# Kernel optimization log

Measured on AMD Instinct MI355X. Metric: run time of the kernel, lower is better.

Reference implementation:

```python
import jax, jax.numpy as jnp
import numpy as np

GRID_SIZE = 5
SPLINE_ORDER = 3
EPS = 1e-5


def make_grid(in_features):
    # efficient-kan: grid_range=[-1,1], points from -order..grid_size+order
    h = 2.0 / GRID_SIZE
    g = jnp.arange(-SPLINE_ORDER, GRID_SIZE + SPLINE_ORDER + 1, dtype=jnp.float32) * h - 1.0
    return jnp.tile(g[None, :], (in_features, 1))  # [in, grid_size + 2*order + 1]


def b_splines(x, grid):
    # x: [B, in], grid: [in, G] -> bases: [B, in, grid_size + order]
    xg = x[:, :, None]
    bases = ((xg >= grid[:, :-1]) & (xg < grid[:, 1:])).astype(x.dtype)
    for k in range(1, SPLINE_ORDER + 1):
        left = (xg - grid[:, : -(k + 1)]) / (grid[:, k:-1] - grid[:, : -(k + 1)])
        right = (grid[:, k + 1:] - xg) / (grid[:, k + 1:] - grid[:, 1:-k])
        bases = left * bases[:, :, :-1] + right * bases[:, :, 1:]
    return bases


def kan_linear(x, grid, base_w, spline_w, spline_scaler):
    # base path: silu(x) @ base_w.T ; spline path: bsplines(x) contracted with scaled spline weight
    base_out = jnp.einsum('bi,oi->bo', jax.nn.silu(x), base_w)
    bases = b_splines(x, grid)  # [B, in, C]
    sw = spline_w * spline_scaler[:, :, None]  # [out, in, C]
    spline_out = jnp.einsum('bic,oic->bo', bases, sw)
    return base_out + spline_out


def layer_norm(x, w, b):
    mu = jnp.mean(x, axis=-1, keepdims=True)
    var = jnp.mean(jnp.square(x - mu), axis=-1, keepdims=True)
    return (x - mu) * jax.lax.rsqrt(var + EPS) * w + b


def setup_inputs() -> dict:
    key = jax.random.key(0)
    ks = jax.random.split(key, 8)
    B, F, H, E = 65536, 32, 64, 64
    OUT = E * F  # 2048
    C = GRID_SIZE + SPLINE_ORDER  # 8 coeffs per edge
    x = jax.random.normal(ks[0], (B, F), dtype=jnp.float32)
    return {
        'x': x,
        'ln_w': jnp.ones((F,), jnp.float32),
        'ln_b': jnp.zeros((F,), jnp.float32),
        'bw1': jax.random.normal(ks[1], (H, F), jnp.float32) * 0.1,
        'sw1': jax.random.normal(ks[2], (H, F, C), jnp.float32) * 0.1,
        'ss1': jax.random.normal(ks[3], (H, F), jnp.float32) * 0.1 + 1.0,
        'bw2': jax.random.normal(ks[4], (OUT, H), jnp.float32) * 0.1,
        'sw2': jax.random.normal(ks[5], (OUT, H, C), jnp.float32) * 0.1,
        'ss2': jax.random.normal(ks[6], (OUT, H), jnp.float32) * 0.1 + 1.0,
        'grid1': make_grid(F),
        'grid2': make_grid(H),
    }


def reference(x, ln_w, ln_b, bw1, sw1, ss1, bw2, sw2, ss2, grid1, grid2):
    h = layer_norm(x, ln_w, ln_b)
    h = kan_linear(h, grid1, bw1, sw1, ss1)   # [B, 64]
    out = kan_linear(h, grid2, bw2, sw2, ss2)  # [B, 2048]
    return out
```

## Files before the change

### kernel.cpp

```cpp
#include <hip/hip_runtime.h>
#include <stdint.h>

#define BATCH   65536
#define FIN     32
#define HID     64
#define NOUT    2048
#define NC      8
#define NF      9
#define K1      288
#define K2      576

#define BM      256
#define BN      256
#define BK      32
#define KT      18
#define NBUF    4

typedef __bf16 bf16x8 __attribute__((ext_vector_type(8)));
typedef float f32x4 __attribute__((ext_vector_type(4)));

__device__ __forceinline__ uint16_t f2bf(float f) {
    uint32_t u = __builtin_bit_cast(uint32_t, f);
    uint32_t r = (u + 0x7fffu + ((u >> 16) & 1u)) >> 16;
    return (uint16_t)r;
}
__device__ __forceinline__ float silu_f(float v) {
    return v / (1.f + __expf(-v));
}

__device__ __forceinline__ void bspline8u(float xv, float out[8]) {
    float s = (xv + 2.2f) * 2.5f;
    int c = (int)floorf(s);
    float gc = (float)(c - 3) * 0.4f - 1.0f;
    float u = (xv - gc) * 2.5f;
    float u1 = 1.f - u;
    float uu = u * u, u3 = uu * u;
    float w0 = u1 * u1 * u1 * (1.f / 6.f);
    float w1 = (3.f * u3 - 6.f * uu + 4.f) * (1.f / 6.f);
    float w2 = (-3.f * u3 + 3.f * uu + 3.f * u + 1.f) * (1.f / 6.f);
    float w3 = u3 * (1.f / 6.f);
#pragma unroll
    for (int t = 0; t < 8; t++) {
        int d = c - t;
        out[t] = (d == 0) ? w3 : (d == 1) ? w2 : (d == 2) ? w1 : (d == 3) ? w0 : 0.f;
    }
}

__global__ void pack_w1(const float* __restrict__ bw1, const float* __restrict__ sw1,
                        const float* __restrict__ ss1, uint16_t* __restrict__ w1L) {
    int idx = blockIdx.x * 256 + threadIdx.x;
    if (idx >= 64 * K1) return;
    int o = idx / K1, k = idx % K1;
    int i = k / 9, j = k % 9;
    float v = (j == 0) ? bw1[o * FIN + i]
                       : sw1[(o * FIN + i) * NC + (j - 1)] * ss1[o * FIN + i];
    w1L[idx] = f2bf(v);
}

__global__ void pack_w2(const float* __restrict__ bw2, const float* __restrict__ sw2,
                        const float* __restrict__ ss2, uint16_t* __restrict__ w2p) {
    int idx = blockIdx.x * 256 + threadIdx.x;
    if (idx >= NOUT * K2) return;
    int n = idx / K2, k = idx % K2;
    int j = k >> 6, i = k & 63;
    float v = (j == 0) ? bw2[n * HID + i]
                       : sw2[(n * HID + i) * NC + (j - 1)] * ss2[n * HID + i];
    w2p[idx] = f2bf(v);
}

#define FBR   64
#define A1LD  296
__global__ __launch_bounds__(256) void featurize(
    const float* __restrict__ x, const float* __restrict__ lnw, const float* __restrict__ lnb,
    const uint16_t* __restrict__ w1L, uint16_t* __restrict__ a2) {

    __shared__ __align__(16) uint16_t w1s[64 * A1LD];
    __shared__ __align__(16) uint16_t a1s[FBR * A1LD];

    const int tid = threadIdx.x;
    const int wv = tid >> 6, lane = tid & 63;
    const int rowBase = blockIdx.x * FBR;

#pragma unroll
    for (int t = 0; t < 9; ++t) {
        int idx = t * 256 + tid;
        int o = idx / 36, cc = idx % 36;
        uint4 v = *(const uint4*)(w1L + idx * 8);
        *(uint4*)&w1s[o * A1LD + cc * 8] = v;
    }

    const int prow = tid >> 2, pq = tid & 3;
    const float* xp = x + (size_t)(rowBase + prow) * FIN + pq * 8;
    float xv[8];
    *(float4*)&xv[0] = ((const float4*)xp)[0];
    *(float4*)&xv[4] = ((const float4*)xp)[1];
    float s = 0.f, s2 = 0.f;
#pragma unroll
    for (int j = 0; j < 8; j++) { s += xv[j]; s2 += xv[j] * xv[j]; }
    s += __shfl_xor(s, 1);  s2 += __shfl_xor(s2, 1);
    s += __shfl_xor(s, 2);  s2 += __shfl_xor(s2, 2);
    const float mu = s * (1.f / 32.f);
    const float var = s2 * (1.f / 32.f) - mu * mu;
    const float rstd = rsqrtf(var + 1e-5f);

    float wl[8], bl[8];
    *(float4*)&wl[0] = ((const float4*)(lnw + pq * 8))[0];
    *(float4*)&wl[4] = ((const float4*)(lnw + pq * 8))[1];
    *(float4*)&bl[0] = ((const float4*)(lnb + pq * 8))[0];
    *(float4*)&bl[4] = ((const float4*)(lnb + pq * 8))[1];

    __align__(16) uint16_t tmp[72];
#pragma unroll
    for (int ii = 0; ii < 8; ii++) {
        float xn = (xv[ii] - mu) * rstd * wl[ii] + bl[ii];
        tmp[ii * 9] = f2bf(silu_f(xn));
        float bs[8];
        bspline8u(xn, bs);
#pragma unroll
        for (int j = 0; j < 8; j++) tmp[ii * 9 + 1 + j] = f2bf(bs[j]);
    }
    {
        uint16_t* dst = &a1s[prow * A1LD + pq * 72];
#pragma unroll
        for (int q = 0; q < 9; q++) *(uint4*)(dst + q * 8) = *(const uint4*)&tmp[q * 8];
    }
    __syncthreads();

    f32x4 acc[4];
#pragma unroll
    for (int n = 0; n < 4; n++) acc[n] = (f32x4){0.f, 0.f, 0.f, 0.f};
    const int arow = wv * 16 + (lane & 15);
    const int koff = (lane >> 4) * 8;
#pragma unroll
    for (int ks = 0; ks < 9; ++ks) {
        bf16x8 af = *(const bf16x8*)&a1s[arow * A1LD + ks * 32 + koff];
#pragma unroll
        for (int n = 0; n < 4; n++) {
            bf16x8 bv = *(const bf16x8*)&w1s[(n * 16 + (lane & 15)) * A1LD + ks * 32 + koff];
            acc[n] = __builtin_amdgcn_mfma_f32_16x16x32_bf16(af, bv, acc[n], 0, 0, 0);
        }
    }

    const int r0 = wv * 16 + ((lane >> 4) << 2);
    const int cb = lane & 15;
#pragma unroll
    for (int n = 0; n < 4; n++)
#pragma unroll
        for (int r = 0; r < 4; r++) {
            float h = acc[n][r];
            float o9[9];
            o9[0] = silu_f(h);
            bspline8u(h, &o9[1]);
            uint16_t* op = a2 + (size_t)(rowBase + r0 + r) * K2 + n * 16 + cb;
#pragma unroll
            for (int j = 0; j < 9; j++) op[j * 64] = f2bf(o9[j]);
        }
}

__device__ __forceinline__ void gload16(const uint16_t* g, const uint16_t* l) {
    __builtin_amdgcn_global_load_lds(
        (const __attribute__((address_space(1))) void*)g,
        (__attribute__((address_space(3))) void*)l, 16, 0, 0);
}

__global__ __launch_bounds__(512, 2) void gemm2_kernel(const uint16_t* __restrict__ A,
                                                       const uint16_t* __restrict__ Bt,
                                                       float* __restrict__ C) {
    __shared__ __align__(16) uint16_t lds[NBUF][2][BM * BK];

    const int tid = threadIdx.x;
    const int wv = tid >> 6, lane = tid & 63;
    const int wr = wv >> 2, wc = wv & 3;

    const uint32_t bid = blockIdx.x;
    const uint32_t wk = (bid & 7u) * 256u + (bid >> 3);
    const uint32_t ntile = wk & 7u, mtile = wk >> 3;

    const int srow = tid >> 2;
    const int scol = (((tid & 3) ^ ((tid >> 3) & 3)) << 3);
    const uint16_t* gA = A  + (size_t)(mtile * BM + srow) * K2 + scol;
    const uint16_t* gB = Bt + (size_t)(ntile * BN + srow) * K2 + scol;

#define STAGE_A(b, kt) do { \
    gload16(gA + (kt) * BK,                    &lds[b][0][wv * 512]); \
    gload16(gA + (size_t)128 * K2 + (kt) * BK, &lds[b][0][4096 + wv * 512]); } while (0)
#define STAGE_B(b, kt) do { \
    gload16(gB + (kt) * BK,                    &lds[b][1][wv * 512]); \
    gload16(gB + (size_t)128 * K2 + (kt) * BK, &lds[b][1][4096 + wv * 512]); } while (0)

    const int slot8 = (((lane >> 4) ^ ((lane >> 1) & 3)) << 3);
    const int aoff = (wr * 128 + (lane & 15)) * BK + slot8;
    const int boff = (wc * 64  + (lane & 15)) * BK + slot8;

    f32x4 acc[8][4];
#pragma unroll
    for (int m = 0; m < 8; m++)
#pragma unroll
        for (int n = 0; n < 4; n++) acc[m][n] = (f32x4){0.f, 0.f, 0.f, 0.f};

    STAGE_A(0, 0); STAGE_B(0, 0);
    STAGE_A(1, 1); STAGE_B(1, 1);
    STAGE_A(2, 2); STAGE_B(2, 2);
    asm volatile("s_waitcnt vmcnt(8)" ::: "memory");
    asm volatile("s_barrier" ::: "memory");

    bf16x8 bvc[4];
#pragma unroll
    for (int n = 0; n < 4; ++n) bvc[n] = *(const bf16x8*)&lds[0][1][boff + n * 512];

#pragma unroll
    for (int t = 0; t < KT; ++t) {
        const int b = t & 3;
        bf16x8 afc[4], afB[4], bvn[4];

#pragma unroll
        for (int m = 0; m < 4; ++m) afc[m] = *(const bf16x8*)&lds[b][0][aoff + m * 512];
#pragma unroll
        for (int m = 0; m < 4; ++m) afB[m] = *(const bf16x8*)&lds[b][0][aoff + (m + 4) * 512];
        if (t + 3 < KT) STAGE_A((t + 3) & 3, t + 3);
        if (t <= KT - 4)      asm volatile("s_waitcnt vmcnt(6)" ::: "memory");
        else if (t == KT - 3) asm volatile("s_waitcnt vmcnt(4)" ::: "memory");
        else if (t == KT - 2) asm volatile("s_waitcnt vmcnt(0)" ::: "memory");
        asm volatile("s_barrier" ::: "memory");

        __builtin_amdgcn_s_setprio(1);
#pragma unroll
        for (int m = 0; m < 4; ++m)
#pragma unroll
            for (int n = 0; n < 4; ++n)
                acc[m][n] = __builtin_amdgcn_mfma_f32_16x16x32_bf16(afc[m], bvc[n], acc[m][n], 0, 0, 0);
        __builtin_amdgcn_s_setprio(0);
        asm volatile("s_barrier" ::: "memory");

        if (t < KT - 1) {
#pragma unroll
            for (int n = 0; n < 4; ++n)
                bvn[n] = *(const bf16x8*)&lds[(t + 1) & 3][1][boff + n * 512];
        }
        if (t + 3 < KT) STAGE_B((t + 3) & 3, t + 3);
        asm volatile("s_barrier" ::: "memory");

        __builtin_amdgcn_s_setprio(1);
#pragma unroll
        for (int m = 0; m < 4; ++m)
#pragma unroll
            for (int n = 0; n < 4; ++n)
                acc[m + 4][n] = __builtin_amdgcn_mfma_f32_16x16x32_bf16(afB[m], bvc[n], acc[m + 4][n], 0, 0, 0);
        __builtin_amdgcn_s_setprio(0);

        if (t < KT - 1) {
            asm volatile("s_barrier" ::: "memory");
#pragma unroll
            for (int n = 0; n < 4; ++n) bvc[n] = bvn[n];
        }
    }
#undef STAGE_A
#undef STAGE_B

    const int crow0 = (int)mtile * BM + wr * 128 + ((lane >> 4) << 2);
    const int ccol0 = (int)ntile * BN + wc * 64 + (lane & 15);
#pragma unroll
    for (int m = 0; m < 8; ++m)
#pragma unroll
        for (int n = 0; n < 4; ++n) {
            float* cp = C + (size_t)(crow0 + m * 16) * NOUT + ccol0 + n * 16;
#pragma unroll
            for (int r = 0; r < 4; ++r) cp[(size_t)r * NOUT] = acc[m][n][r];
        }
}

extern "C" void kernel_launch(void* const* d_in, const int* in_sizes, int n_in,
                              void* d_out, int out_size, void* d_ws, size_t ws_size,
                              hipStream_t stream) {
    const float* x    = (const float*)d_in[0];
    const float* lnw  = (const float*)d_in[1];
    const float* lnb  = (const float*)d_in[2];
    const float* bw1  = (const float*)d_in[3];
    const float* sw1  = (const float*)d_in[4];
    const float* ss1  = (const float*)d_in[5];
    const float* bw2  = (const float*)d_in[6];
    const float* sw2  = (const float*)d_in[7];
    const float* ss2  = (const float*)d_in[8];

    char* ws = (char*)d_ws;
    uint16_t* w1L = (uint16_t*)ws;
    uint16_t* w2p = (uint16_t*)(ws + 65536);
    uint16_t* a2  = (uint16_t*)(ws + 65536 + 2359296);
    float* out = (float*)d_out;

    pack_w1<<<dim3(72), dim3(256), 0, stream>>>(bw1, sw1, ss1, w1L);
    pack_w2<<<dim3((NOUT * K2 + 255) / 256), dim3(256), 0, stream>>>(bw2, sw2, ss2, w2p);
    featurize<<<dim3(BATCH / FBR), dim3(256), 0, stream>>>(x, lnw, lnb, w1L, a2);
    gemm2_kernel<<<dim3((BATCH / BM) * (NOUT / BN)), dim3(512), 0, stream>>>(a2, w2p, out);
}
```

Measured before the change: 282.4 us.

## Stage featurize output through LDS and rework GEMM into four interleaved MFMA phases

The featurize kernel now writes its second-layer features into a shared-memory tile that reuses the weight buffer, then copies whole rows to global memory with 16-byte stores instead of scattered 2-byte stores. The GEMM main loop is split into four phases per K-step. Each phase loads two A fragments, issues one global-to-LDS load, and runs eight MFMAs. The B-fragment double buffering in registers is removed to cut register pressure. This adds more barriers and lgkmcnt waits per iteration, which could stall the MFMA pipe.

```diff
diff --git a/kernel.cpp b/kernel.cpp
--- a/kernel.cpp
+++ b/kernel.cpp
@@ -68,14 +68,17 @@
     w2p[idx] = f2bf(v);
 }
 
-#define FBR   64
-#define A1LD  296
+#define FBR    64
+#define A1LD   296
+#define S2LD   584
 __global__ __launch_bounds__(256) void featurize(
     const float* __restrict__ x, const float* __restrict__ lnw, const float* __restrict__ lnb,
     const uint16_t* __restrict__ w1L, uint16_t* __restrict__ a2) {
 
-    __shared__ __align__(16) uint16_t w1s[64 * A1LD];
-    __shared__ __align__(16) uint16_t a1s[FBR * A1LD];
+    __shared__ __align__(16) char fsm[75776];
+    uint16_t* w1s = (uint16_t*)fsm;
+    uint16_t* a1s = (uint16_t*)(fsm + 37888);
+    uint16_t* s2  = (uint16_t*)fsm;
 
     const int tid = threadIdx.x;
     const int wv = tid >> 6, lane = tid & 63;
@@ -94,13 +97,13 @@
     float xv[8];
     *(float4*)&xv[0] = ((const float4*)xp)[0];
     *(float4*)&xv[4] = ((const float4*)xp)[1];
-    float s = 0.f, s2 = 0.f;
-#pragma unroll
-    for (int j = 0; j < 8; j++) { s += xv[j]; s2 += xv[j] * xv[j]; }
-    s += __shfl_xor(s, 1);  s2 += __shfl_xor(s2, 1);
-    s += __shfl_xor(s, 2);  s2 += __shfl_xor(s2, 2);
+    float s = 0.f, s2v = 0.f;
+#pragma unroll
+    for (int j = 0; j < 8; j++) { s += xv[j]; s2v += xv[j] * xv[j]; }
+    s += __shfl_xor(s, 1);  s2v += __shfl_xor(s2v, 1);
+    s += __shfl_xor(s, 2);  s2v += __shfl_xor(s2v, 2);
     const float mu = s * (1.f / 32.f);
-    const float var = s2 * (1.f / 32.f) - mu * mu;
+    const float var = s2v * (1.f / 32.f) - mu * mu;
     const float rstd = rsqrtf(var + 1e-5f);
 
     float wl[8], bl[8];
@@ -140,6 +143,7 @@
             acc[n] = __builtin_amdgcn_mfma_f32_16x16x32_bf16(af, bv, acc[n], 0, 0, 0);
         }
     }
+    __syncthreads();
 
     const int r0 = wv * 16 + ((lane >> 4) << 2);
     const int cb = lane & 15;
@@ -151,10 +155,19 @@
             float o9[9];
             o9[0] = silu_f(h);
             bspline8u(h, &o9[1]);
-            uint16_t* op = a2 + (size_t)(rowBase + r0 + r) * K2 + n * 16 + cb;
+            uint16_t* op = &s2[(size_t)(r0 + r) * S2LD + n * 16 + cb];
 #pragma unroll
             for (int j = 0; j < 9; j++) op[j * 64] = f2bf(o9[j]);
         }
+    __syncthreads();
+
+#pragma unroll
+    for (int q = 0; q < 18; ++q) {
+        int g = q * 256 + tid;
+        int row = g / 72, c = g % 72;
+        uint4 v = *(const uint4*)&s2[row * S2LD + c * 8];
+        *(uint4*)(a2 + (size_t)(rowBase + row) * K2 + c * 8) = v;
+    }
 }
 
 __device__ __forceinline__ void gload16(const uint16_t* g, const uint16_t* l) {
@@ -181,13 +194,6 @@
     const uint16_t* gA = A  + (size_t)(mtile * BM + srow) * K2 + scol;
     const uint16_t* gB = Bt + (size_t)(ntile * BN + srow) * K2 + scol;
 
-#define STAGE_A(b, kt) do { \
-    gload16(gA + (kt) * BK,                    &lds[b][0][wv * 512]); \
-    gload16(gA + (size_t)128 * K2 + (kt) * BK, &lds[b][0][4096 + wv * 512]); } while (0)
-#define STAGE_B(b, kt) do { \
-    gload16(gB + (kt) * BK,                    &lds[b][1][wv * 512]); \
-    gload16(gB + (size_t)128 * K2 + (kt) * BK, &lds[b][1][4096 + wv * 512]); } while (0)
-
     const int slot8 = (((lane >> 4) ^ ((lane >> 1) & 3)) << 3);
     const int aoff = (wr * 128 + (lane & 15)) * BK + slot8;
     const int boff = (wc * 64  + (lane & 15)) * BK + slot8;
@@ -198,64 +204,91 @@
 #pragma unroll
         for (int n = 0; n < 4; n++) acc[m][n] = (f32x4){0.f, 0.f, 0.f, 0.f};
 
-    STAGE_A(0, 0); STAGE_B(0, 0);
-    STAGE_A(1, 1); STAGE_B(1, 1);
-    STAGE_A(2, 2); STAGE_B(2, 2);
+#define ST_A0(b, kt) gload16(gA + (kt) * BK,                    &lds[b][0][wv * 512])
+#define ST_A1(b, kt) gload16(gA + (size_t)128 * K2 + (kt) * BK, &lds[b][0][4096 + wv * 512])
+#define ST_B0(b, kt) gload16(gB + (kt) * BK,                    &lds[b][1][wv * 512])
+#define ST_B1(b, kt) gload16(gB + (size_t)128 * K2 + (kt) * BK, &lds[b][1][4096 + wv * 512])
+
+    ST_A0(0, 0); ST_A1(0, 0); ST_B0(0, 0); ST_B1(0, 0);
+    ST_A0(1, 1); ST_A1(1, 1); ST_B0(1, 1); ST_B1(1, 1);
+    ST_A0(2, 2); ST_A1(2, 2); ST_B0(2, 2); ST_B1(2, 2);
     asm volatile("s_waitcnt vmcnt(8)" ::: "memory");
     asm volatile("s_barrier" ::: "memory");
 
-    bf16x8 bvc[4];
-#pragma unroll
-    for (int n = 0; n < 4; ++n) bvc[n] = *(const bf16x8*)&lds[0][1][boff + n * 512];
-
 #pragma unroll
     for (int t = 0; t < KT; ++t) {
         const int b = t & 3;
-        bf16x8 afc[4], afB[4], bvn[4];
-
-#pragma unroll
-        for (int m = 0; m < 4; ++m) afc[m] = *(const bf16x8*)&lds[b][0][aoff + m * 512];
-#pragma unroll
-        for (int m = 0; m < 4; ++m) afB[m] = *(const bf16x8*)&lds[b][0][aoff + (m + 4) * 512];
-        if (t + 3 < KT) STAGE_A((t + 3) & 3, t + 3);
-        if (t <= KT - 4)      asm volatile("s_waitcnt vmcnt(6)" ::: "memory");
+        const int nb = (t + 3) & 3;
+        const bool st = (t + 3 < KT);
+        const uint16_t* As = &lds[b][0][0];
+        const uint16_t* Bs = &lds[b][1][0];
+        bf16x8 bv[4], aa, ab;
+
+#pragma unroll
+        for (int n = 0; n < 4; ++n) bv[n] = *(const bf16x8*)&Bs[boff + n * 512];
+        aa = *(const bf16x8*)&As[aoff];
+        ab = *(const bf16x8*)&As[aoff + 512];
+        if (st) ST_A0(nb, t + 3);
+        asm volatile("s_barrier" ::: "memory");
+        asm volatile("s_waitcnt lgkmcnt(0)" ::: "memory");
+        __builtin_amdgcn_sched_barrier(0);
+        __builtin_amdgcn_s_setprio(1);
+#pragma unroll
+        for (int n = 0; n < 4; ++n) acc[0][n] = __builtin_amdgcn_mfma_f32_16x16x32_bf16(aa, bv[n], acc[0][n], 0, 0, 0);
+#pragma unroll
+        for (int n = 0; n < 4; ++n) acc[1][n] = __builtin_amdgcn_mfma_f32_16x16x32_bf16(ab, bv[n], acc[1][n], 0, 0, 0);
+        __builtin_amdgcn_s_setprio(0);
+        asm volatile("s_barrier" ::: "memory");
+
+        aa = *(const bf16x8*)&As[aoff + 2 * 512];
+        ab = *(const bf16x8*)&As[aoff + 3 * 512];
+        if (st) ST_A1(nb, t + 3);
+        asm volatile("s_barrier" ::: "memory");
+        asm volatile("s_waitcnt lgkmcnt(0)" ::: "memory");
+        __builtin_amdgcn_sched_barrier(0);
+        __builtin_amdgcn_s_setprio(1);
+#pragma unroll
+        for (int n = 0; n < 4; ++n) acc[2][n] = __builtin_amdgcn_mfma_f32_16x16x32_bf16(aa, bv[n], acc[2][n], 0, 0, 0);
+#pragma unroll
+        for (int n = 0; n < 4; ++n) acc[3][n] = __builtin_amdgcn_mfma_f32_16x16x32_bf16(ab, bv[n], acc[3][n], 0, 0, 0);
+        __builtin_amdgcn_s_setprio(0);
+        asm volatile("s_barrier" ::: "memory");
+
+        aa = *(const bf16x8*)&As[aoff + 4 * 512];
+        ab = *(const bf16x8*)&As[aoff + 5 * 512];
+        if (st) ST_B0(nb, t + 3);
+        asm volatile("s_barrier" ::: "memory");
+        asm volatile("s_waitcnt lgkmcnt(0)" ::: "memory");
+        __builtin_amdgcn_sched_barrier(0);
+        __builtin_amdgcn_s_setprio(1);
+#pragma unroll
+        for (int n = 0; n < 4; ++n) acc[4][n] = __builtin_amdgcn_mfma_f32_16x16x32_bf16(aa, bv[n], acc[4][n], 0, 0, 0);
+#pragma unroll
+        for (int n = 0; n < 4; ++n) acc[5][n] = __builtin_amdgcn_mfma_f32_16x16x32_bf16(ab, bv[n], acc[5][n], 0, 0, 0);
+        __builtin_amdgcn_s_setprio(0);
+        asm volatile("s_barrier" ::: "memory");
+
+        aa = *(const bf16x8*)&As[aoff + 6 * 512];
+        ab = *(const bf16x8*)&As[aoff + 7 * 512];
+        if (st) ST_B1(nb, t + 3);
+        asm volatile("s_barrier" ::: "memory");
+        asm volatile("s_waitcnt lgkmcnt(0)" ::: "memory");
+        __builtin_amdgcn_sched_barrier(0);
+        __builtin_amdgcn_s_setprio(1);
+#pragma unroll
+        for (int n = 0; n < 4; ++n) acc[6][n] = __builtin_amdgcn_mfma_f32_16x16x32_bf16(aa, bv[n], acc[6][n], 0, 0, 0);
+#pragma unroll
+        for (int n = 0; n < 4; ++n) acc[7][n] = __builtin_amdgcn_mfma_f32_16x16x32_bf16(ab, bv[n], acc[7][n], 0, 0, 0);
+        __builtin_amdgcn_s_setprio(0);
+        if (t <= KT - 4)      asm volatile("s_waitcnt vmcnt(8)" ::: "memory");
         else if (t == KT - 3) asm volatile("s_waitcnt vmcnt(4)" ::: "memory");
         else if (t == KT - 2) asm volatile("s_waitcnt vmcnt(0)" ::: "memory");
-        asm volatile("s_barrier" ::: "memory");
-
-        __builtin_amdgcn_s_setprio(1);
-#pragma unroll
-        for (int m = 0; m < 4; ++m)
-#pragma unroll
-            for (int n = 0; n < 4; ++n)
-                acc[m][n] = __builtin_amdgcn_mfma_f32_16x16x32_bf16(afc[m], bvc[n], acc[m][n], 0, 0, 0);
-        __builtin_amdgcn_s_setprio(0);
-        asm volatile("s_barrier" ::: "memory");
-
-        if (t < KT - 1) {
-#pragma unroll
-            for (int n = 0; n < 4; ++n)
-                bvn[n] = *(const bf16x8*)&lds[(t + 1) & 3][1][boff + n * 512];
-        }
-        if (t + 3 < KT) STAGE_B((t + 3) & 3, t + 3);
-        asm volatile("s_barrier" ::: "memory");
-
-        __builtin_amdgcn_s_setprio(1);
-#pragma unroll
-        for (int m = 0; m < 4; ++m)
-#pragma unroll
-            for (int n = 0; n < 4; ++n)
-                acc[m + 4][n] = __builtin_amdgcn_mfma_f32_16x16x32_bf16(afB[m], bvc[n], acc[m + 4][n], 0, 0, 0);
-        __builtin_amdgcn_s_setprio(0);
-
-        if (t < KT - 1) {
-            asm volatile("s_barrier" ::: "memory");
-#pragma unroll
-            for (int n = 0; n < 4; ++n) bvc[n] = bvn[n];
-        }
-    }
-#undef STAGE_A
-#undef STAGE_B
+        if (t < KT - 1) asm volatile("s_barrier" ::: "memory");
+    }
+#undef ST_A0
+#undef ST_A1
+#undef ST_B0
+#undef ST_B1
 
     const int crow0 = (int)mtile * BM + wr * 128 + ((lane >> 4) << 2);
     const int ccol0 = (int)ntile * BN + wc * 64 + (lane & 15);
```

New measurement: 291.6 us. +3.3%, slower.

## Quantize second-layer GEMM to int8 with per-row and per-column scales

Applied to the files above, without the earlier changes.

Replaces the bf16 second GEMM with an int8 MFMA GEMM (16x16x64 i8), quantizing weights per output column and activations per batch row using max-abs scaling. The activation quantization is fused into featurize and goes through LDS to produce coalesced int8 stores. Scales are applied in the epilogue. This halves operand bytes and doubles MFMA throughput per instruction, but int8 quantization of spline/silu features may exceed the accuracy tolerance.

```diff
diff --git a/kernel.cpp b/kernel.cpp
--- a/kernel.cpp
+++ b/kernel.cpp
@@ -10,14 +10,12 @@
 #define K1      288
 #define K2      576
 
-#define BM      256
-#define BN      256
-#define BK      32
-#define KT      18
-#define NBUF    4
+#define BKI     64
+#define KTI     9
 
 typedef __bf16 bf16x8 __attribute__((ext_vector_type(8)));
 typedef float f32x4 __attribute__((ext_vector_type(4)));
+typedef int   i32x4 __attribute__((ext_vector_type(4)));
 
 __device__ __forceinline__ uint16_t f2bf(float f) {
     uint32_t u = __builtin_bit_cast(uint32_t, f);
@@ -57,25 +55,41 @@
     w1L[idx] = f2bf(v);
 }
 
-__global__ void pack_w2(const float* __restrict__ bw2, const float* __restrict__ sw2,
-                        const float* __restrict__ ss2, uint16_t* __restrict__ w2p) {
-    int idx = blockIdx.x * 256 + threadIdx.x;
-    if (idx >= NOUT * K2) return;
-    int n = idx / K2, k = idx % K2;
-    int j = k >> 6, i = k & 63;
-    float v = (j == 0) ? bw2[n * HID + i]
-                       : sw2[(n * HID + i) * NC + (j - 1)] * ss2[n * HID + i];
-    w2p[idx] = f2bf(v);
-}
-
-#define FBR   64
-#define A1LD  296
+__global__ void pack_w2i(const float* __restrict__ bw2, const float* __restrict__ sw2,
+                         const float* __restrict__ ss2, int8_t* __restrict__ w2i,
+                         float* __restrict__ sb) {
+    int gid = blockIdx.x * 256 + threadIdx.x;
+    int o = gid >> 6, lane = gid & 63;
+    float v[9];
+    float mx = 1e-20f;
+#pragma unroll
+    for (int j = 0; j < 9; j++) {
+        int k = lane * 9 + j;
+        int jj = k >> 6, i = k & 63;
+        v[j] = (jj == 0) ? bw2[o * HID + i]
+                         : sw2[(o * HID + i) * NC + (jj - 1)] * ss2[o * HID + i];
+        mx = fmaxf(mx, fabsf(v[j]));
+    }
+#pragma unroll
+    for (int m = 1; m < 64; m <<= 1) mx = fmaxf(mx, __shfl_xor(mx, m));
+    float qs = 127.f / mx;
+    if (lane == 0) sb[o] = mx * (1.f / 127.f);
+#pragma unroll
+    for (int j = 0; j < 9; j++)
+        w2i[(size_t)o * K2 + lane * 9 + j] = (int8_t)(int)rintf(v[j] * qs);
+}
+
+#define FBR    64
+#define A1LD   296
+#define S2BLD  592
 __global__ __launch_bounds__(256) void featurize(
     const float* __restrict__ x, const float* __restrict__ lnw, const float* __restrict__ lnb,
-    const uint16_t* __restrict__ w1L, uint16_t* __restrict__ a2) {
-
-    __shared__ __align__(16) uint16_t w1s[64 * A1LD];
-    __shared__ __align__(16) uint16_t a1s[FBR * A1LD];
+    const uint16_t* __restrict__ w1L, int8_t* __restrict__ a2i, float* __restrict__ sa) {
+
+    __shared__ __align__(16) char fsm[75776];
+    uint16_t* w1s = (uint16_t*)fsm;
+    uint16_t* a1s = (uint16_t*)(fsm + 37888);
+    int8_t*   s2b = (int8_t*)fsm;
 
     const int tid = threadIdx.x;
     const int wv = tid >> 6, lane = tid & 63;
@@ -94,13 +108,13 @@
     float xv[8];
     *(float4*)&xv[0] = ((const float4*)xp)[0];
     *(float4*)&xv[4] = ((const float4*)xp)[1];
-    float s = 0.f, s2 = 0.f;
-#pragma unroll
-    for (int j = 0; j < 8; j++) { s += xv[j]; s2 += xv[j] * xv[j]; }
-    s += __shfl_xor(s, 1);  s2 += __shfl_xor(s2, 1);
-    s += __shfl_xor(s, 2);  s2 += __shfl_xor(s2, 2);
+    float s = 0.f, s2v = 0.f;
+#pragma unroll
+    for (int j = 0; j < 8; j++) { s += xv[j]; s2v += xv[j] * xv[j]; }
+    s += __shfl_xor(s, 1);  s2v += __shfl_xor(s2v, 1);
+    s += __shfl_xor(s, 2);  s2v += __shfl_xor(s2v, 2);
     const float mu = s * (1.f / 32.f);
-    const float var = s2 * (1.f / 32.f) - mu * mu;
+    const float var = s2v * (1.f / 32.f) - mu * mu;
     const float rstd = rsqrtf(var + 1e-5f);
 
     float wl[8], bl[8];
@@ -140,9 +154,11 @@
             acc[n] = __builtin_amdgcn_mfma_f32_16x16x32_bf16(af, bv, acc[n], 0, 0, 0);
         }
     }
+    __syncthreads();
 
     const int r0 = wv * 16 + ((lane >> 4) << 2);
     const int cb = lane & 15;
+    float rmax[4] = {1e-20f, 1e-20f, 1e-20f, 1e-20f};
 #pragma unroll
     for (int n = 0; n < 4; n++)
 #pragma unroll
@@ -151,22 +167,57 @@
             float o9[9];
             o9[0] = silu_f(h);
             bspline8u(h, &o9[1]);
-            uint16_t* op = a2 + (size_t)(rowBase + r0 + r) * K2 + n * 16 + cb;
-#pragma unroll
-            for (int j = 0; j < 9; j++) op[j * 64] = f2bf(o9[j]);
-        }
-}
-
-__device__ __forceinline__ void gload16(const uint16_t* g, const uint16_t* l) {
+            float mx = fabsf(o9[0]);
+#pragma unroll
+            for (int j = 1; j < 9; j++) mx = fmaxf(mx, fabsf(o9[j]));
+            rmax[r] = fmaxf(rmax[r], mx);
+        }
+#pragma unroll
+    for (int m = 1; m < 16; m <<= 1)
+#pragma unroll
+        for (int r = 0; r < 4; r++) rmax[r] = fmaxf(rmax[r], __shfl_xor(rmax[r], m));
+    float qs[4];
+#pragma unroll
+    for (int r = 0; r < 4; r++) qs[r] = 127.f / rmax[r];
+    if (cb == 0)
+#pragma unroll
+        for (int r = 0; r < 4; r++) sa[rowBase + r0 + r] = rmax[r] * (1.f / 127.f);
+
+#pragma unroll
+    for (int n = 0; n < 4; n++)
+#pragma unroll
+        for (int r = 0; r < 4; r++) {
+            float h = acc[n][r];
+            float o9[9];
+            o9[0] = silu_f(h);
+            bspline8u(h, &o9[1]);
+            int8_t* op = &s2b[(r0 + r) * S2BLD + n * 16 + cb];
+#pragma unroll
+            for (int j = 0; j < 9; j++) op[j * 64] = (int8_t)(int)rintf(o9[j] * qs[r]);
+        }
+    __syncthreads();
+
+#pragma unroll
+    for (int q = 0; q < 9; ++q) {
+        int g = q * 256 + tid;
+        int row = g / 36, c = g % 36;
+        uint4 v = *(const uint4*)&s2b[row * S2BLD + c * 16];
+        *(uint4*)(a2i + (size_t)(rowBase + row) * K2 + c * 16) = v;
+    }
+}
+
+__device__ __forceinline__ void gload16(const void* g, const void* l) {
     __builtin_amdgcn_global_load_lds(
         (const __attribute__((address_space(1))) void*)g,
         (__attribute__((address_space(3))) void*)l, 16, 0, 0);
 }
 
-__global__ __launch_bounds__(512, 2) void gemm2_kernel(const uint16_t* __restrict__ A,
-                                                       const uint16_t* __restrict__ Bt,
-                                                       float* __restrict__ C) {
-    __shared__ __align__(16) uint16_t lds[NBUF][2][BM * BK];
+__global__ __launch_bounds__(512, 2) void gemm2i(const int8_t* __restrict__ A,
+                                                 const int8_t* __restrict__ Bt,
+                                                 const float* __restrict__ sa,
+                                                 const float* __restrict__ sb,
+                                                 float* __restrict__ C) {
+    __shared__ __align__(16) int8_t lds[4][2][256 * BKI];
 
     const int tid = threadIdx.x;
     const int wv = tid >> 6, lane = tid & 63;
@@ -177,26 +228,26 @@
     const uint32_t ntile = wk & 7u, mtile = wk >> 3;
 
     const int srow = tid >> 2;
-    const int scol = (((tid & 3) ^ ((tid >> 3) & 3)) << 3);
-    const uint16_t* gA = A  + (size_t)(mtile * BM + srow) * K2 + scol;
-    const uint16_t* gB = Bt + (size_t)(ntile * BN + srow) * K2 + scol;
+    const int scol = (((tid & 3) ^ ((tid >> 4) & 3)) << 4);
+    const int8_t* gA = A  + (size_t)(mtile * 256 + srow) * K2 + scol;
+    const int8_t* gB = Bt + (size_t)(ntile * 256 + srow) * K2 + scol;
 
 #define STAGE_A(b, kt) do { \
-    gload16(gA + (kt) * BK,                    &lds[b][0][wv * 512]); \
-    gload16(gA + (size_t)128 * K2 + (kt) * BK, &lds[b][0][4096 + wv * 512]); } while (0)
+    gload16(gA + (kt) * BKI,                    &lds[b][0][wv * 1024]); \
+    gload16(gA + (size_t)128 * K2 + (kt) * BKI, &lds[b][0][8192 + wv * 1024]); } while (0)
 #define STAGE_B(b, kt) do { \
-    gload16(gB + (kt) * BK,                    &lds[b][1][wv * 512]); \
-    gload16(gB + (size_t)128 * K2 + (kt) * BK, &lds[b][1][4096 + wv * 512]); } while (0)
-
-    const int slot8 = (((lane >> 4) ^ ((lane >> 1) & 3)) << 3);
-    const int aoff = (wr * 128 + (lane & 15)) * BK + slot8;
-    const int boff = (wc * 64  + (lane & 15)) * BK + slot8;
-
-    f32x4 acc[8][4];
+    gload16(gB + (kt) * BKI,                    &lds[b][1][wv * 1024]); \
+    gload16(gB + (size_t)128 * K2 + (kt) * BKI, &lds[b][1][8192 + wv * 1024]); } while (0)
+
+    const int slot16 = (((lane >> 4) ^ ((lane >> 2) & 3)) << 4);
+    const int aoff = (wr * 128 + (lane & 15)) * BKI + slot16;
+    const int boff = (wc * 64  + (lane & 15)) * BKI + slot16;
+
+    i32x4 acc[8][4];
 #pragma unroll
     for (int m = 0; m < 8; m++)
 #pragma unroll
-        for (int n = 0; n < 4; n++) acc[m][n] = (f32x4){0.f, 0.f, 0.f, 0.f};
+        for (int n = 0; n < 4; n++) acc[m][n] = (i32x4){0, 0, 0, 0};
 
     STAGE_A(0, 0); STAGE_B(0, 0);
     STAGE_A(1, 1); STAGE_B(1, 1);
@@ -204,23 +255,23 @@
     asm volatile("s_waitcnt vmcnt(8)" ::: "memory");
     asm volatile("s_barrier" ::: "memory");
 
-    bf16x8 bvc[4];
-#pragma unroll
-    for (int n = 0; n < 4; ++n) bvc[n] = *(const bf16x8*)&lds[0][1][boff + n * 512];
-
-#pragma unroll
-    for (int t = 0; t < KT; ++t) {
+    i32x4 bvc[4];
+#pragma unroll
+    for (int n = 0; n < 4; ++n) bvc[n] = *(const i32x4*)&lds[0][1][boff + n * 1024];
+
+#pragma unroll
+    for (int t = 0; t < KTI; ++t) {
         const int b = t & 3;
-        bf16x8 afc[4], afB[4], bvn[4];
-
-#pragma unroll
-        for (int m = 0; m < 4; ++m) afc[m] = *(const bf16x8*)&lds[b][0][aoff + m * 512];
-#pragma unroll
-        for (int m = 0; m < 4; ++m) afB[m] = *(const bf16x8*)&lds[b][0][aoff + (m + 4) * 512];
-        if (t + 3 < KT) STAGE_A((t + 3) & 3, t + 3);
-        if (t <= KT - 4)      asm volatile("s_waitcnt vmcnt(6)" ::: "memory");
-        else if (t == KT - 3) asm volatile("s_waitcnt vmcnt(4)" ::: "memory");
-        else if (t == KT - 2) asm volatile("s_waitcnt vmcnt(0)" ::: "memory");
+        i32x4 afc[4], afB[4], bvn[4];
+
+#pragma unroll
+        for (int m = 0; m < 4; ++m) afc[m] = *(const i32x4*)&lds[b][0][aoff + m * 1024];
+#pragma unroll
+        for (int m = 0; m < 4; ++m) afB[m] = *(const i32x4*)&lds[b][0][aoff + (m + 4) * 1024];
+        if (t + 3 < KTI) STAGE_A((t + 3) & 3, t + 3);
+        if (t <= KTI - 4)      asm volatile("s_waitcnt vmcnt(6)" ::: "memory");
+        else if (t == KTI - 3) asm volatile("s_waitcnt vmcnt(4)" ::: "memory");
+        else if (t == KTI - 2) asm volatile("s_waitcnt vmcnt(0)" ::: "memory");
         asm volatile("s_barrier" ::: "memory");
 
         __builtin_amdgcn_s_setprio(1);
@@ -228,16 +279,16 @@
         for (int m = 0; m < 4; ++m)
 #pragma unroll
             for (int n = 0; n < 4; ++n)
-                acc[m][n] = __builtin_amdgcn_mfma_f32_16x16x32_bf16(afc[m], bvc[n], acc[m][n], 0, 0, 0);
+                acc[m][n] = __builtin_amdgcn_mfma_i32_16x16x64_i8(afc[m], bvc[n], acc[m][n], 0, 0, 0);
         __builtin_amdgcn_s_setprio(0);
         asm volatile("s_barrier" ::: "memory");
 
-        if (t < KT - 1) {
+        if (t < KTI - 1) {
 #pragma unroll
             for (int n = 0; n < 4; ++n)
-                bvn[n] = *(const bf16x8*)&lds[(t + 1) & 3][1][boff + n * 512];
-        }
-        if (t + 3 < KT) STAGE_B((t + 3) & 3, t + 3);
+                bvn[n] = *(const i32x4*)&lds[(t + 1) & 3][1][boff + n * 1024];
+        }
+        if (t + 3 < KTI) STAGE_B((t + 3) & 3, t + 3);
         asm volatile("s_barrier" ::: "memory");
 
         __builtin_amdgcn_s_setprio(1);
@@ -245,10 +296,10 @@
         for (int m = 0; m < 4; ++m)
 #pragma unroll
             for (int n = 0; n < 4; ++n)
-                acc[m + 4][n] = __builtin_amdgcn_mfma_f32_16x16x32_bf16(afB[m], bvc[n], acc[m + 4][n], 0, 0, 0);
+                acc[m + 4][n] = __builtin_amdgcn_mfma_i32_16x16x64_i8(afB[m], bvc[n], acc[m + 4][n], 0, 0, 0);
         __builtin_amdgcn_s_setprio(0);
 
-        if (t < KT - 1) {
+        if (t < KTI - 1) {
             asm volatile("s_barrier" ::: "memory");
 #pragma unroll
             for (int n = 0; n < 4; ++n) bvc[n] = bvn[n];
@@ -257,16 +308,24 @@
 #undef STAGE_A
 #undef STAGE_B
 
-    const int crow0 = (int)mtile * BM + wr * 128 + ((lane >> 4) << 2);
-    const int ccol0 = (int)ntile * BN + wc * 64 + (lane & 15);
-#pragma unroll
-    for (int m = 0; m < 8; ++m)
+    const int crow0 = (int)mtile * 256 + wr * 128 + ((lane >> 4) << 2);
+    const int ccol0 = (int)ntile * 256 + wc * 64 + (lane & 15);
+    float sbv[4];
+#pragma unroll
+    for (int n = 0; n < 4; ++n) sbv[n] = sb[ccol0 + n * 16];
+#pragma unroll
+    for (int m = 0; m < 8; ++m) {
+        float sav[4];
+#pragma unroll
+        for (int r = 0; r < 4; ++r) sav[r] = sa[crow0 + m * 16 + r];
 #pragma unroll
         for (int n = 0; n < 4; ++n) {
             float* cp = C + (size_t)(crow0 + m * 16) * NOUT + ccol0 + n * 16;
 #pragma unroll
-            for (int r = 0; r < 4; ++r) cp[(size_t)r * NOUT] = acc[m][n][r];
-        }
+            for (int r = 0; r < 4; ++r)
+                cp[(size_t)r * NOUT] = (float)acc[m][n][r] * sav[r] * sbv[n];
+        }
+    }
 }
 
 extern "C" void kernel_launch(void* const* d_in, const int* in_sizes, int n_in,
@@ -284,12 +343,14 @@
 
     char* ws = (char*)d_ws;
     uint16_t* w1L = (uint16_t*)ws;
-    uint16_t* w2p = (uint16_t*)(ws + 65536);
-    uint16_t* a2  = (uint16_t*)(ws + 65536 + 2359296);
+    int8_t*   w2i = (int8_t*)(ws + 65536);
+    float*    sb  = (float*)(ws + 1310720);
+    float*    sa  = (float*)(ws + 1376256);
+    int8_t*   a2i = (int8_t*)(ws + 1703936);
     float* out = (float*)d_out;
 
     pack_w1<<<dim3(72), dim3(256), 0, stream>>>(bw1, sw1, ss1, w1L);
-    pack_w2<<<dim3((NOUT * K2 + 255) / 256), dim3(256), 0, stream>>>(bw2, sw2, ss2, w2p);
-    featurize<<<dim3(BATCH / FBR), dim3(256), 0, stream>>>(x, lnw, lnb, w1L, a2);
-    gemm2_kernel<<<dim3((BATCH / BM) * (NOUT / BN)), dim3(512), 0, stream>>>(a2, w2p, out);
-}
+    pack_w2i<<<dim3(NOUT / 4), dim3(256), 0, stream>>>(bw2, sw2, ss2, w2i, sb);
+    featurize<<<dim3(BATCH / FBR), dim3(256), 0, stream>>>(x, lnw, lnb, w1L, a2i, sa);
+    gemm2i<<<dim3((BATCH / 256) * (NOUT / 256)), dim3(512), 0, stream>>>(a2i, w2i, sa, sb, out);
+}
```

New measurement: 378.7 us. 34.1% more time.

## Switch GEMM to 32x32x16 MFMA and stage featurize output through LDS

Applied to the files above, without the earlier changes.

The main GEMM now uses 32x32x16 bf16 MFMA tiles with 16-float accumulators instead of 16x16x32. This cuts LDS fragment reads per MFMA and simplifies the barrier and prefetch schedule by dropping the B-fragment double buffering. Featurize now writes its second-layer activations into shared memory and copies them out as coalesced 16-byte row stores instead of scattered 2-byte global writes. The costs are an extra LDS round trip and barriers in featurize, and a more strided accumulator store pattern in the GEMM epilogue.

```diff
diff --git a/kernel.cpp b/kernel.cpp
--- a/kernel.cpp
+++ b/kernel.cpp
@@ -10,14 +10,12 @@
 #define K1      288
 #define K2      576
 
-#define BM      256
-#define BN      256
 #define BK      32
 #define KT      18
-#define NBUF    4
 
 typedef __bf16 bf16x8 __attribute__((ext_vector_type(8)));
-typedef float f32x4 __attribute__((ext_vector_type(4)));
+typedef float f32x4  __attribute__((ext_vector_type(4)));
+typedef float f32x16 __attribute__((ext_vector_type(16)));
 
 __device__ __forceinline__ uint16_t f2bf(float f) {
     uint32_t u = __builtin_bit_cast(uint32_t, f);
@@ -68,14 +66,17 @@
     w2p[idx] = f2bf(v);
 }
 
-#define FBR   64
-#define A1LD  296
+#define FBR    64
+#define A1LD   296
+#define S2LD   584
 __global__ __launch_bounds__(256) void featurize(
     const float* __restrict__ x, const float* __restrict__ lnw, const float* __restrict__ lnb,
     const uint16_t* __restrict__ w1L, uint16_t* __restrict__ a2) {
 
-    __shared__ __align__(16) uint16_t w1s[64 * A1LD];
-    __shared__ __align__(16) uint16_t a1s[FBR * A1LD];
+    __shared__ __align__(16) char fsm[75776];
+    uint16_t* w1s = (uint16_t*)fsm;
+    uint16_t* a1s = (uint16_t*)(fsm + 37888);
+    uint16_t* s2  = (uint16_t*)fsm;
 
     const int tid = threadIdx.x;
     const int wv = tid >> 6, lane = tid & 63;
@@ -94,13 +95,13 @@
     float xv[8];
     *(float4*)&xv[0] = ((const float4*)xp)[0];
     *(float4*)&xv[4] = ((const float4*)xp)[1];
-    float s = 0.f, s2 = 0.f;
-#pragma unroll
-    for (int j = 0; j < 8; j++) { s += xv[j]; s2 += xv[j] * xv[j]; }
-    s += __shfl_xor(s, 1);  s2 += __shfl_xor(s2, 1);
-    s += __shfl_xor(s, 2);  s2 += __shfl_xor(s2, 2);
+    float s = 0.f, s2v = 0.f;
+#pragma unroll
+    for (int j = 0; j < 8; j++) { s += xv[j]; s2v += xv[j] * xv[j]; }
+    s += __shfl_xor(s, 1);  s2v += __shfl_xor(s2v, 1);
+    s += __shfl_xor(s, 2);  s2v += __shfl_xor(s2v, 2);
     const float mu = s * (1.f / 32.f);
-    const float var = s2 * (1.f / 32.f) - mu * mu;
+    const float var = s2v * (1.f / 32.f) - mu * mu;
     const float rstd = rsqrtf(var + 1e-5f);
 
     float wl[8], bl[8];
@@ -140,6 +141,7 @@
             acc[n] = __builtin_amdgcn_mfma_f32_16x16x32_bf16(af, bv, acc[n], 0, 0, 0);
         }
     }
+    __syncthreads();
 
     const int r0 = wv * 16 + ((lane >> 4) << 2);
     const int cb = lane & 15;
@@ -151,10 +153,19 @@
             float o9[9];
             o9[0] = silu_f(h);
             bspline8u(h, &o9[1]);
-            uint16_t* op = a2 + (size_t)(rowBase + r0 + r) * K2 + n * 16 + cb;
+            uint16_t* op = &s2[(size_t)(r0 + r) * S2LD + n * 16 + cb];
 #pragma unroll
             for (int j = 0; j < 9; j++) op[j * 64] = f2bf(o9[j]);
         }
+    __syncthreads();
+
+#pragma unroll
+    for (int q = 0; q < 18; ++q) {
+        int g = q * 256 + tid;
+        int row = g / 72, c = g % 72;
+        uint4 v = *(const uint4*)&s2[row * S2LD + c * 8];
+        *(uint4*)(a2 + (size_t)(rowBase + row) * K2 + c * 8) = v;
+    }
 }
 
 __device__ __forceinline__ void gload16(const uint16_t* g, const uint16_t* l) {
@@ -166,7 +177,7 @@
 __global__ __launch_bounds__(512, 2) void gemm2_kernel(const uint16_t* __restrict__ A,
                                                        const uint16_t* __restrict__ Bt,
                                                        float* __restrict__ C) {
-    __shared__ __align__(16) uint16_t lds[NBUF][2][BM * BK];
+    __shared__ __align__(16) uint16_t lds[4][2][256 * BK];
 
     const int tid = threadIdx.x;
     const int wv = tid >> 6, lane = tid & 63;
@@ -178,8 +189,8 @@
 
     const int srow = tid >> 2;
     const int scol = (((tid & 3) ^ ((tid >> 3) & 3)) << 3);
-    const uint16_t* gA = A  + (size_t)(mtile * BM + srow) * K2 + scol;
-    const uint16_t* gB = Bt + (size_t)(ntile * BN + srow) * K2 + scol;
+    const uint16_t* gA = A  + (size_t)(mtile * 256 + srow) * K2 + scol;
+    const uint16_t* gB = Bt + (size_t)(ntile * 256 + srow) * K2 + scol;
 
 #define STAGE_A(b, kt) do { \
     gload16(gA + (kt) * BK,                    &lds[b][0][wv * 512]); \
@@ -188,15 +199,21 @@
     gload16(gB + (kt) * BK,                    &lds[b][1][wv * 512]); \
     gload16(gB + (size_t)128 * K2 + (kt) * BK, &lds[b][1][4096 + wv * 512]); } while (0)
 
-    const int slot8 = (((lane >> 4) ^ ((lane >> 1) & 3)) << 3);
-    const int aoff = (wr * 128 + (lane & 15)) * BK + slot8;
-    const int boff = (wc * 64  + (lane & 15)) * BK + slot8;
-
-    f32x4 acc[8][4];
-#pragma unroll
-    for (int m = 0; m < 8; m++)
-#pragma unroll
-        for (int n = 0; n < 4; n++) acc[m][n] = (f32x4){0.f, 0.f, 0.f, 0.f};
+    const int r5 = lane & 31;
+    const int kg = lane >> 5;
+    const int sx = (lane >> 1) & 3;
+    const int swzK0 = ((kg    ) ^ sx) << 3;
+    const int swzK1 = ((kg | 2) ^ sx) << 3;
+    const int abase = (wr * 128 + r5) * BK;
+    const int bbase = (wc * 64  + r5) * BK;
+
+    f32x16 acc[4][2];
+#pragma unroll
+    for (int m = 0; m < 4; m++)
+#pragma unroll
+        for (int n = 0; n < 2; n++)
+#pragma unroll
+            for (int r = 0; r < 16; r++) acc[m][n][r] = 0.f;
 
     STAGE_A(0, 0); STAGE_B(0, 0);
     STAGE_A(1, 1); STAGE_B(1, 1);
@@ -204,19 +221,23 @@
     asm volatile("s_waitcnt vmcnt(8)" ::: "memory");
     asm volatile("s_barrier" ::: "memory");
 
-    bf16x8 bvc[4];
-#pragma unroll
-    for (int n = 0; n < 4; ++n) bvc[n] = *(const bf16x8*)&lds[0][1][boff + n * 512];
-
 #pragma unroll
     for (int t = 0; t < KT; ++t) {
         const int b = t & 3;
-        bf16x8 afc[4], afB[4], bvn[4];
-
-#pragma unroll
-        for (int m = 0; m < 4; ++m) afc[m] = *(const bf16x8*)&lds[b][0][aoff + m * 512];
-#pragma unroll
-        for (int m = 0; m < 4; ++m) afB[m] = *(const bf16x8*)&lds[b][0][aoff + (m + 4) * 512];
+        const uint16_t* As = &lds[b][0][0];
+        const uint16_t* Bs = &lds[b][1][0];
+        bf16x8 bv[2][2], af[2][2], ag[2][2];
+
+#pragma unroll
+        for (int n = 0; n < 2; ++n) {
+            bv[n][0] = *(const bf16x8*)&Bs[bbase + n * 1024 + swzK0];
+            bv[n][1] = *(const bf16x8*)&Bs[bbase + n * 1024 + swzK1];
+        }
+#pragma unroll
+        for (int m = 0; m < 2; ++m) {
+            af[m][0] = *(const bf16x8*)&As[abase + m * 1024 + swzK0];
+            af[m][1] = *(const bf16x8*)&As[abase + m * 1024 + swzK1];
+        }
         if (t + 3 < KT) STAGE_A((t + 3) & 3, t + 3);
         if (t <= KT - 4)      asm volatile("s_waitcnt vmcnt(6)" ::: "memory");
         else if (t == KT - 3) asm volatile("s_waitcnt vmcnt(4)" ::: "memory");
@@ -225,47 +246,45 @@
 
         __builtin_amdgcn_s_setprio(1);
 #pragma unroll
-        for (int m = 0; m < 4; ++m)
-#pragma unroll
-            for (int n = 0; n < 4; ++n)
-                acc[m][n] = __builtin_amdgcn_mfma_f32_16x16x32_bf16(afc[m], bvc[n], acc[m][n], 0, 0, 0);
+        for (int m = 0; m < 2; ++m)
+#pragma unroll
+            for (int n = 0; n < 2; ++n)
+#pragma unroll
+                for (int ks = 0; ks < 2; ++ks)
+                    acc[m][n] = __builtin_amdgcn_mfma_f32_32x32x16_bf16(af[m][ks], bv[n][ks], acc[m][n], 0, 0, 0);
         __builtin_amdgcn_s_setprio(0);
         asm volatile("s_barrier" ::: "memory");
 
-        if (t < KT - 1) {
-#pragma unroll
-            for (int n = 0; n < 4; ++n)
-                bvn[n] = *(const bf16x8*)&lds[(t + 1) & 3][1][boff + n * 512];
+#pragma unroll
+        for (int m = 0; m < 2; ++m) {
+            ag[m][0] = *(const bf16x8*)&As[abase + (m + 2) * 1024 + swzK0];
+            ag[m][1] = *(const bf16x8*)&As[abase + (m + 2) * 1024 + swzK1];
         }
         if (t + 3 < KT) STAGE_B((t + 3) & 3, t + 3);
-        asm volatile("s_barrier" ::: "memory");
-
         __builtin_amdgcn_s_setprio(1);
 #pragma unroll
-        for (int m = 0; m < 4; ++m)
-#pragma unroll
-            for (int n = 0; n < 4; ++n)
-                acc[m + 4][n] = __builtin_amdgcn_mfma_f32_16x16x32_bf16(afB[m], bvc[n], acc[m + 4][n], 0, 0, 0);
+        for (int m = 0; m < 2; ++m)
+#pragma unroll
+            for (int n = 0; n < 2; ++n)
+#pragma unroll
+                for (int ks = 0; ks < 2; ++ks)
+                    acc[m + 2][n] = __builtin_amdgcn_mfma_f32_32x32x16_bf16(ag[m][ks], bv[n][ks], acc[m + 2][n], 0, 0, 0);
         __builtin_amdgcn_s_setprio(0);
-
-        if (t < KT - 1) {
-            asm volatile("s_barrier" ::: "memory");
-#pragma unroll
-            for (int n = 0; n < 4; ++n) bvc[n] = bvn[n];
-        }
+        if (t < KT - 1) asm volatile("s_barrier" ::: "memory");
     }
 #undef STAGE_A
 #undef STAGE_B
 
-    const int crow0 = (int)mtile * BM + wr * 128 + ((lane >> 4) << 2);
-    const int ccol0 = (int)ntile * BN + wc * 64 + (lane & 15);
-#pragma unroll
-    for (int m = 0; m < 8; ++m)
-#pragma unroll
-        for (int n = 0; n < 4; ++n) {
-            float* cp = C + (size_t)(crow0 + m * 16) * NOUT + ccol0 + n * 16;
-#pragma unroll
-            for (int r = 0; r < 4; ++r) cp[(size_t)r * NOUT] = acc[m][n][r];
+    const int ccolb = (int)ntile * 256 + wc * 64 + r5;
+    const int crowb = (int)mtile * 256 + wr * 128 + 4 * kg;
+#pragma unroll
+    for (int m = 0; m < 4; ++m)
+#pragma unroll
+        for (int n = 0; n < 2; ++n) {
+            float* cp = C + (size_t)(crowb + m * 32) * NOUT + ccolb + n * 32;
+#pragma unroll
+            for (int r = 0; r < 16; ++r)
+                cp[(size_t)((r & 3) + 8 * (r >> 2)) * NOUT] = acc[m][n][r];
         }
 }
 
@@ -291,5 +310,5 @@
     pack_w1<<<dim3(72), dim3(256), 0, stream>>>(bw1, sw1, ss1, w1L);
     pack_w2<<<dim3((NOUT * K2 + 255) / 256), dim3(256), 0, stream>>>(bw2, sw2, ss2, w2p);
     featurize<<<dim3(BATCH / FBR), dim3(256), 0, stream>>>(x, lnw, lnb, w1L, a2);
-    gemm2_kernel<<<dim3((BATCH / BM) * (NOUT / BN)), dim3(512), 0, stream>>>(a2, w2p, out);
-}
+    gemm2_kernel<<<dim3((BATCH / 256) * (NOUT / 256)), dim3(512), 0, stream>>>(a2, w2p, out);
+}
```

Measured after the change: 300.3 us. +6.4%, slower.
